# Performance work log

Measured on AMD Instinct MI355X. Metric: run time of the kernel, lower is better.

The kernel has to match this reference:

```python
import jax, jax.numpy as jnp
import numpy as np

N_SRC, N_DST, E, D, H = 100000, 10000, 320000, 128, 128
LN_EPS = 1e-5


def setup_inputs() -> dict:
    key = jax.random.key(0)
    ks = jax.random.split(key, 12)
    h_src = jax.random.normal(ks[0], (N_SRC, D), jnp.float32)
    h_dst = jax.random.normal(ks[1], (N_DST, D), jnp.float32)
    s_emb = jax.random.normal(ks[2], (N_DST, D), jnp.float32)
    edge_weight = jax.random.uniform(ks[3], (E,), jnp.float32)
    src_idx = jax.random.randint(ks[4], (E,), 0, N_SRC)
    dst_idx = jnp.sort(jax.random.randint(ks[5], (E,), 0, N_DST))
    # session_attention: Linear(2D->H, no bias) -> tanh -> Linear(H->1, no bias)
    W1 = jax.random.normal(ks[6], (2 * D, H), jnp.float32) / np.sqrt(2 * D)
    w2 = jax.random.normal(ks[7], (H,), jnp.float32) / np.sqrt(H)
    # output_proj: Linear(2D->D) with bias
    Wo = jax.random.normal(ks[8], (2 * D, D), jnp.float32) / np.sqrt(2 * D)
    bo = jnp.zeros((D,), jnp.float32)
    gamma = jnp.ones((D,), jnp.float32)
    beta = jnp.zeros((D,), jnp.float32)
    return {"h_src": h_src, "h_dst": h_dst, "s_emb": s_emb,
            "edge_weight": edge_weight, "src_idx": src_idx, "dst_idx": dst_idx,
            "W1": W1, "w2": w2, "Wo": Wo, "bo": bo, "gamma": gamma, "beta": beta}


def reference(h_src, h_dst, s_emb, edge_weight, src_idx, dst_idx, W1, w2, Wo, bo, gamma, beta):
    d = h_src.shape[1]
    # concat([h_src[src], s_emb[dst]]) @ W1 == h_src[src] @ W1[:d] + s_emb[dst] @ W1[d:]
    # project per-node first (cheaper than per-edge concat matmul)
    p_src = h_src @ W1[:d]          # [N_src, H]
    p_dst = s_emb @ W1[d:]          # [N_dst, H]
    raw = jnp.tanh(p_src[src_idx] + p_dst[dst_idx]) @ w2   # [E]
    raw = raw * edge_weight
    # edge_softmax: segment softmax over incoming edges of each dst node
    seg_max = jax.ops.segment_max(raw, dst_idx, num_segments=h_dst.shape[0])
    seg_max = jnp.where(jnp.isfinite(seg_max), seg_max, 0.0)  # handle degree-0 dsts
    ex = jnp.exp(raw - seg_max[dst_idx])
    den = jax.ops.segment_sum(ex, dst_idx, num_segments=h_dst.shape[0])
    attn = ex / den[dst_idx]                                 # [E]
    # u_mul_e + sum: weighted gather-scatter aggregation
    h_global = jax.ops.segment_sum(h_src[src_idx] * attn[:, None], dst_idx,
                                   num_segments=h_dst.shape[0])  # [N_dst, D]
    # output_proj on concat([h_dst, h_global])
    out = h_dst @ Wo[:d] + h_global @ Wo[d:] + bo
    # residual + layer norm (dropout = identity in eval)
    x = h_dst + out
    mu = jnp.mean(x, axis=-1, keepdims=True)
    var = jnp.mean((x - mu) ** 2, axis=-1, keepdims=True)
    y = (x - mu) / jnp.sqrt(var + LN_EPS) * gamma + beta
    return (y, attn[:, None])
```

## Files before the change

### kernel.cpp

```cpp
#include <hip/hip_runtime.h>
#include <math.h>

#define D128 128
#define SCAPW 256

typedef unsigned int uint32;
typedef unsigned short ushort_t;
typedef short bf16x8 __attribute__((ext_vector_type(8)));
typedef float f32x4 __attribute__((ext_vector_type(4)));
typedef float f32x2 __attribute__((ext_vector_type(2)));

__device__ __forceinline__ ushort_t bf16_of(float x) {
  uint32 u = __float_as_uint(x);
  return (ushort_t)((u + 0x7fffu + ((u >> 16) & 1u)) >> 16);
}
__device__ __forceinline__ uint32 pack_bf2(float x, float y) {
  uint32 bx = __float_as_uint(x);
  uint32 by = __float_as_uint(y);
  bx = (bx + 0x7fffu + ((bx >> 16) & 1u)) >> 16;
  by = (by + 0x7fffu + ((by >> 16) & 1u)) & 0xffff0000u;
  return bx | by;
}
__device__ __forceinline__ float bf_lo(uint32 u) { return __uint_as_float(u << 16); }
__device__ __forceinline__ float bf_hi(uint32 u) { return __uint_as_float(u & 0xffff0000u); }

__device__ __forceinline__ float fast_tanh(float x) {
  float e = __expf(2.0f * x);
  float r = __builtin_amdgcn_rcpf(1.0f + e);
  return fmaf(-2.0f, r, 1.0f);
}

__device__ __forceinline__ uint32 pack_fp8x4(float a, float b, float c, float d) {
  int u = __builtin_amdgcn_cvt_pk_fp8_f32(a, b, 0, false);
  u = __builtin_amdgcn_cvt_pk_fp8_f32(c, d, u, true);
  return (uint32)u;
}

__global__ __launch_bounds__(256) void prep_all(
    const float* __restrict__ h_src, const float* __restrict__ s_emb,
    const float* __restrict__ h_dst,
    const float* __restrict__ W1, const float* __restrict__ Wo,
    const int* __restrict__ dst_idx,
    uint32* __restrict__ h_src_bf, uint32* __restrict__ s_emb_bf,
    uint32* __restrict__ h_dst_bf, uint32* __restrict__ h_src_f8,
    ushort_t* __restrict__ Wfrag, ushort_t* __restrict__ Wo_frag,
    int* __restrict__ off,
    int n_src_el, int n_dst_el, int E, int N, int nb_conv) {
  const int b = blockIdx.x;
  const int tid = threadIdx.x;
  if (b < nb_conv) {
    int i = (b * 256 + tid) * 8;
    if (i < n_src_el) {
      float4 a = *(const float4*)(h_src + i);
      float4 c = *(const float4*)(h_src + i + 4);
      uint4 p;
      p.x = pack_bf2(a.x, a.y);
      p.y = pack_bf2(a.z, a.w);
      p.z = pack_bf2(c.x, c.y);
      p.w = pack_bf2(c.z, c.w);
      *(uint4*)(h_src_bf + (i >> 1)) = p;
      uint2 q;
      q.x = pack_fp8x4(a.x, a.y, a.z, a.w);
      q.y = pack_fp8x4(c.x, c.y, c.z, c.w);
      *(uint2*)(h_src_f8 + (i >> 2)) = q;
    } else if (i < n_src_el + 2 * n_dst_el) {
      const float* src;
      uint32* dst;
      if (i < n_src_el + n_dst_el) {
        src = s_emb + (i - n_src_el); dst = s_emb_bf + ((i - n_src_el) >> 1);
      } else {
        src = h_dst + (i - n_src_el - n_dst_el);
        dst = h_dst_bf + ((i - n_src_el - n_dst_el) >> 1);
      }
      float4 a = *(const float4*)src;
      float4 c = *(const float4*)(src + 4);
      uint4 p;
      p.x = pack_bf2(a.x, a.y);
      p.y = pack_bf2(a.z, a.w);
      p.z = pack_bf2(c.x, c.y);
      p.w = pack_bf2(c.z, c.w);
      *(uint4*)dst = p;
    }
  } else if (b < nb_conv + 16) {
    int t = (b - nb_conv) * 256 + tid;
    int lane = t & 63;
    int kc = (t >> 6) & 3;
    int nt = (t >> 8) & 7;
    int h = (t >> 11) & 1;
    int m = lane & 15;
    int quad = lane >> 4;
    int krow = h * D128 + kc * 32 + quad * 8;
    int ncol = nt * 16 + m;
    ushort_t fr[8];
#pragma unroll
    for (int j = 0; j < 8; j++) fr[j] = bf16_of(W1[(size_t)(krow + j) * D128 + ncol]);
    *(uint4*)(Wfrag + (size_t)t * 8) = *(const uint4*)fr;
  } else if (b < nb_conv + 32) {
    int t = (b - nb_conv - 16) * 256 + tid;
    int lane = t & 63;
    int kc = (t >> 6) & 7;
    int nt = (t >> 9) & 7;
    int m = lane & 15;
    int quad = lane >> 4;
    int krow = kc * 32 + quad * 8;
    int ncol = nt * 16 + m;
    ushort_t fr[8];
#pragma unroll
    for (int j = 0; j < 8; j++) fr[j] = bf16_of(Wo[(size_t)(krow + j) * D128 + ncol]);
    *(uint4*)(Wo_frag + (size_t)t * 8) = *(const uint4*)fr;
  } else {
    int e = (b - nb_conv - 32) * 256 + tid;
    if (e >= E) return;
    int d = dst_idx[e];
    int dprev = (e == 0) ? -1 : dst_idx[e - 1];
    for (int v = dprev + 1; v <= d; v++) off[v] = e;
    if (e == E - 1) {
      for (int v = d + 1; v <= N; v++) off[v] = E;
    }
  }
}

__global__ __launch_bounds__(256) void gemm_mfma(
    const ushort_t* __restrict__ Xa, const ushort_t* __restrict__ Xb,
    const ushort_t* __restrict__ Wfrag,
    uint32* __restrict__ Pa, uint32* __restrict__ Pb,
    int Ma, int Mb, int nblk_a) {
  __shared__ uint32 Ys8[128][36];
  const int blk = blockIdx.x;
  const ushort_t* X;
  const bf16x8* Wf;
  uint32* P;
  int M, row0;
  if (blk < nblk_a) { X = Xa; P = Pa; Wf = (const bf16x8*)Wfrag;           M = Ma; row0 = blk * 128; }
  else              { X = Xb; P = Pb; Wf = (const bf16x8*)(Wfrag + 16384); M = Mb; row0 = (blk - nblk_a) * 128; }

  const int tid = threadIdx.x;
  const int wave = tid >> 6;
  const int lane = tid & 63;
  const int m = lane & 15;
  const int quad = lane >> 4;

  const int ra0 = min(row0 + wave * 32 + m, M - 1);
  const int ra1 = min(row0 + wave * 32 + 16 + m, M - 1);

  f32x4 acc[2][8];
#pragma unroll
  for (int st = 0; st < 2; st++)
#pragma unroll
    for (int nt = 0; nt < 8; nt++) acc[st][nt] = (f32x4){0.f, 0.f, 0.f, 0.f};

#pragma unroll
  for (int kc = 0; kc < 4; kc++) {
    bf16x8 x0 = *(const bf16x8*)(X + (size_t)ra0 * D128 + kc * 32 + quad * 8);
    bf16x8 x1 = *(const bf16x8*)(X + (size_t)ra1 * D128 + kc * 32 + quad * 8);
#pragma unroll
    for (int nt = 0; nt < 8; nt++) {
      bf16x8 wf = Wf[(nt * 4 + kc) * 64 + lane];
      acc[0][nt] = __builtin_amdgcn_mfma_f32_16x16x32_bf16(wf, x0, acc[0][nt], 0, 0, 0);
      acc[1][nt] = __builtin_amdgcn_mfma_f32_16x16x32_bf16(wf, x1, acc[1][nt], 0, 0, 0);
    }
  }

#pragma unroll
  for (int st = 0; st < 2; st++)
#pragma unroll
    for (int nt = 0; nt < 8; nt++)
      Ys8[wave * 32 + st * 16 + m][nt * 4 + quad] =
          pack_fp8x4(acc[st][nt][0], acc[st][nt][1], acc[st][nt][2], acc[st][nt][3]);
  __syncthreads();

#pragma unroll
  for (int it = 0; it < 4; it++) {
    int f = tid + 256 * it;
    int row = f >> 3;
    int cu = (f & 7) * 4;
    int grow = row0 + row;
    if (grow < M) *(uint4*)(P + (size_t)grow * 32 + cu) = *(const uint4*)(&Ys8[row][cu]);
  }
}

__global__ __launch_bounds__(256) void attn_agg_kernel(
    const uint32* __restrict__ p_src_f8, const uint32* __restrict__ p_dst_f8,
    const float* __restrict__ w2, const float* __restrict__ ew,
    const int* __restrict__ src_idx, const int* __restrict__ off,
    const uint32* __restrict__ h_src_f8,
    float* __restrict__ attn_out, uint32* __restrict__ h_glob_bf, int N_dst) {
  const int tid = threadIdx.x;
  const int wv = tid >> 6;
  const int lane = tid & 63;
  const int v = blockIdx.x * 4 + wv;

  __shared__ float sex[4][SCAPW];
  __shared__ int ssrc[4][SCAPW];
  if (v >= N_dst) return;

  const int lo = off[v], hi = off[v + 1];
  const int deg = hi - lo;
  const int sub = lane & 15;
  const int eg = lane >> 4;
  const bool fast = (deg <= SCAPW);

  float4 wA = *(const float4*)(w2 + sub * 8);
  float4 wB = *(const float4*)(w2 + sub * 8 + 4);
  uint2 pdu = *(const uint2*)(p_dst_f8 + (size_t)v * 32 + sub * 2);
  f32x2 pd0 = __builtin_amdgcn_cvt_pk_f32_fp8(pdu.x, false);
  f32x2 pd1 = __builtin_amdgcn_cvt_pk_f32_fp8(pdu.x, true);
  f32x2 pd2 = __builtin_amdgcn_cvt_pk_f32_fp8(pdu.y, false);
  f32x2 pd3 = __builtin_amdgcn_cvt_pk_f32_fp8(pdu.y, true);

  float den = 0.f;
  for (int base = 0; base < deg; base += 4) {
    const int ei = base + eg;
    float ex = 0.f;
    if (ei < deg) {
      const int e = lo + ei;
      const int s = src_idx[e];
      const float ewv = ew[e];
      uint2 us = *(const uint2*)(p_src_f8 + (size_t)s * 32 + sub * 2);
      f32x2 a0 = __builtin_amdgcn_cvt_pk_f32_fp8(us.x, false);
      f32x2 a1 = __builtin_amdgcn_cvt_pk_f32_fp8(us.x, true);
      f32x2 a2 = __builtin_amdgcn_cvt_pk_f32_fp8(us.y, false);
      f32x2 a3 = __builtin_amdgcn_cvt_pk_f32_fp8(us.y, true);
      float sc;
      sc = fast_tanh(a0.x + pd0.x) * wA.x;
      sc = fmaf(fast_tanh(a0.y + pd0.y), wA.y, sc);
      sc = fmaf(fast_tanh(a1.x + pd1.x), wA.z, sc);
      sc = fmaf(fast_tanh(a1.y + pd1.y), wA.w, sc);
      sc = fmaf(fast_tanh(a2.x + pd2.x), wB.x, sc);
      sc = fmaf(fast_tanh(a2.y + pd2.y), wB.y, sc);
      sc = fmaf(fast_tanh(a3.x + pd3.x), wB.z, sc);
      sc = fmaf(fast_tanh(a3.y + pd3.y), wB.w, sc);
#pragma unroll
      for (int o = 1; o <= 8; o <<= 1) sc += __shfl_xor(sc, o, 64);
      ex = __expf(sc * ewv);
      if (sub == 0) {
        if (fast) { sex[wv][ei] = ex; ssrc[wv][ei] = s; }
        else attn_out[lo + ei] = ex;
      }
    }
    den += (sub == 0) ? ex : 0.f;
  }
#pragma unroll
  for (int o = 1; o <= 32; o <<= 1) den += __shfl_xor(den, o, 64);
  const float inv = (deg > 0) ? 1.0f / den : 0.0f;

  const int c4 = lane & 31;
  const int hw = lane >> 5;
  float a0 = 0.f, a1 = 0.f, a2 = 0.f, a3 = 0.f;

  if (fast) {
    const int pad = (deg + 15) & ~15;
    for (int i = deg + lane; i < pad; i += 64) { sex[wv][i] = 0.f; ssrc[wv][i] = 0; }
    for (int i = lane; i < deg; i += 64) attn_out[lo + i] = sex[wv][i] * inv;
    for (int b = 0; b < pad; b += 16) {
#pragma unroll
      for (int j = 0; j < 8; j++) {
        const int idx = b + j * 2 + hw;
        float ex = sex[wv][idx];
        int s = ssrc[wv][idx];
        uint32 u = h_src_f8[(size_t)s * 32 + c4];
        f32x2 h0 = __builtin_amdgcn_cvt_pk_f32_fp8(u, false);
        f32x2 h1 = __builtin_amdgcn_cvt_pk_f32_fp8(u, true);
        a0 = fmaf(ex, h0.x, a0);
        a1 = fmaf(ex, h0.y, a1);
        a2 = fmaf(ex, h1.x, a2);
        a3 = fmaf(ex, h1.y, a3);
      }
    }
  } else {
    for (int b = 0; b < deg; b += 16) {
#pragma unroll
      for (int j = 0; j < 8; j++) {
        const int idx = b + j * 2 + hw;
        float ex = 0.f;
        int s = 0;
        if (idx < deg) { ex = attn_out[lo + idx]; s = src_idx[lo + idx]; }
        uint32 u = h_src_f8[(size_t)s * 32 + c4];
        f32x2 h0 = __builtin_amdgcn_cvt_pk_f32_fp8(u, false);
        f32x2 h1 = __builtin_amdgcn_cvt_pk_f32_fp8(u, true);
        a0 = fmaf(ex, h0.x, a0);
        a1 = fmaf(ex, h0.y, a1);
        a2 = fmaf(ex, h1.x, a2);
        a3 = fmaf(ex, h1.y, a3);
      }
    }
    for (int i = lane; i < deg; i += 64) attn_out[lo + i] *= inv;
  }

  a0 += __shfl_xor(a0, 32, 64);
  a1 += __shfl_xor(a1, 32, 64);
  a2 += __shfl_xor(a2, 32, 64);
  a3 += __shfl_xor(a3, 32, 64);
  if (hw == 0) {
    uint2 o;
    o.x = pack_bf2(a0 * inv, a1 * inv);
    o.y = pack_bf2(a2 * inv, a3 * inv);
    *(uint2*)(h_glob_bf + (size_t)v * 64 + c4 * 2) = o;
  }
}

__global__ __launch_bounds__(128) void out_mfma_ln(
    const ushort_t* __restrict__ h_dst_bf, const ushort_t* __restrict__ h_glob_bf,
    const ushort_t* __restrict__ Wo_frag,
    const float* __restrict__ h_dst, const float* __restrict__ bo,
    const float* __restrict__ gamma, const float* __restrict__ beta,
    float* __restrict__ y, int N) {
  __shared__ float sbo[128], sgam[128], sbet[128];
  const int tid = threadIdx.x;
  if (tid < 128) { sbo[tid] = bo[tid]; sgam[tid] = gamma[tid]; sbet[tid] = beta[tid]; }
  __syncthreads();

  const int w = tid >> 6;
  const int lane = tid & 63;
  const int m = lane & 15;
  const int quad = lane >> 4;
  const int row0 = blockIdx.x * 32 + w * 16;
  const int ra = min(row0 + m, N - 1);
  const bf16x8* Wf = (const bf16x8*)Wo_frag;

  f32x4 acc[8];
#pragma unroll
  for (int nt = 0; nt < 8; nt++) acc[nt] = (f32x4){0.f, 0.f, 0.f, 0.f};

#pragma unroll
  for (int kc = 0; kc < 8; kc++) {
    const ushort_t* X = (kc < 4) ? h_dst_bf : h_glob_bf;
    const int kk = kc & 3;
    bf16x8 a = *(const bf16x8*)(X + (size_t)ra * D128 + kk * 32 + quad * 8);
#pragma unroll
    for (int nt = 0; nt < 8; nt++) {
      bf16x8 bfr = Wf[(nt * 8 + kc) * 64 + lane];
      acc[nt] = __builtin_amdgcn_mfma_f32_16x16x32_bf16(a, bfr, acc[nt], 0, 0, 0);
    }
  }

#pragma unroll
  for (int r = 0; r < 4; r++) {
    const int grow = row0 + quad * 4 + r;
    const int gr = min(grow, N - 1);
    float x[8];
    float s1 = 0.f, s2 = 0.f;
#pragma unroll
    for (int nt = 0; nt < 8; nt++) {
      float hd = h_dst[(size_t)gr * D128 + nt * 16 + m];
      float xv = hd + acc[nt][r] + sbo[nt * 16 + m];
      x[nt] = xv;
      s1 += xv;
      s2 = fmaf(xv, xv, s2);
    }
#pragma unroll
    for (int o = 1; o <= 8; o <<= 1) {
      s1 += __shfl_xor(s1, o, 64);
      s2 += __shfl_xor(s2, o, 64);
    }
    float mu = s1 * (1.0f / 128.0f);
    float var = s2 * (1.0f / 128.0f) - mu * mu;
    float rstd = __builtin_amdgcn_rcpf(sqrtf(var + 1e-5f));
    if (grow < N) {
#pragma unroll
      for (int nt = 0; nt < 8; nt++) {
        int c = nt * 16 + m;
        y[(size_t)grow * D128 + c] = (x[nt] - mu) * rstd * sgam[c] + sbet[c];
      }
    }
  }
}

extern "C" void kernel_launch(void* const* d_in, const int* in_sizes, int n_in,
                              void* d_out, int out_size, void* d_ws, size_t ws_size,
                              hipStream_t stream) {
  const float* h_src = (const float*)d_in[0];
  const float* h_dst = (const float*)d_in[1];
  const float* s_emb = (const float*)d_in[2];
  const float* ew    = (const float*)d_in[3];
  const int* src_idx = (const int*)d_in[4];
  const int* dst_idx = (const int*)d_in[5];
  const float* W1    = (const float*)d_in[6];
  const float* w2    = (const float*)d_in[7];
  const float* Wo    = (const float*)d_in[8];
  const float* bo    = (const float*)d_in[9];
  const float* gamma = (const float*)d_in[10];
  const float* beta  = (const float*)d_in[11];

  const int N_src = in_sizes[0] / D128;
  const int N_dst = in_sizes[1] / D128;
  const int E = in_sizes[3];

  float* out_y = (float*)d_out;
  float* out_attn = out_y + (size_t)N_dst * D128;

  uint32* p_src_f8 = (uint32*)d_ws;
  uint32* p_dst_f8 = p_src_f8 + (size_t)N_src * 32;
  uint32* h_src_f8 = p_dst_f8 + (size_t)N_dst * 32;
  uint32* h_src_bf = h_src_f8 + (size_t)N_src * 32;
  uint32* h_dst_bf = h_src_bf + (size_t)N_src * 64;
  uint32* h_glob_bf = h_dst_bf + (size_t)N_dst * 64;
  uint32* s_emb_bf = h_glob_bf + (size_t)N_dst * 64;
  int* seg_off = (int*)(s_emb_bf + (size_t)N_dst * 64);
  ushort_t* Wfrag = (ushort_t*)(seg_off + N_dst + 1 + 3);
  ushort_t* Wo_frag = Wfrag + 32768;

  const int n_src_el = N_src * D128;
  const int n_dst_el = N_dst * D128;
  const int n_conv_el = n_src_el + 2 * n_dst_el;
  const int nblk_a = (N_src + 127) / 128;
  const int nblk_b = (N_dst + 127) / 128;
  const int nb_conv = (n_conv_el / 8 + 255) / 256;
  const int nb_seg = (E + 255) / 256;

  prep_all<<<nb_conv + 32 + nb_seg, 256, 0, stream>>>(
      h_src, s_emb, h_dst, W1, Wo, dst_idx,
      h_src_bf, s_emb_bf, h_dst_bf, h_src_f8, Wfrag, Wo_frag, seg_off,
      n_src_el, n_dst_el, E, N_dst, nb_conv);
  gemm_mfma<<<nblk_a + nblk_b, 256, 0, stream>>>(
      (const ushort_t*)h_src_bf, (const ushort_t*)s_emb_bf, Wfrag,
      p_src_f8, p_dst_f8, N_src, N_dst, nblk_a);
  attn_agg_kernel<<<(N_dst + 3) / 4, 256, 0, stream>>>(
      p_src_f8, p_dst_f8, w2, ew, src_idx, seg_off, h_src_f8, out_attn,
      h_glob_bf, N_dst);
  out_mfma_ln<<<(N_dst + 31) / 32, 128, 0, stream>>>(
      (const ushort_t*)h_dst_bf, (const ushort_t*)h_glob_bf, Wo_frag,
      h_dst, bo, gamma, beta, out_y, N_dst);
}
```

Baseline: 175.9 us.

## Fuse fp32-to-bf16/fp8 conversion into GEMM and output kernels

Removes the separate conversion pass in prep_all that wrote bf16 copies of h_src, s_emb and h_dst and an fp8 copy of h_src. The GEMM now reads fp32 inputs directly, converts them to bf16 in registers, and also emits the fp8 h_src copy. The output projection converts h_dst on the fly. This removes a full read-write round trip over about 60 MB of activations, in exchange for twice the input bytes per GEMM load and conversion ALU work inside the MFMA kernels.

```diff
diff --git a/kernel.cpp b/kernel.cpp
--- a/kernel.cpp
+++ b/kernel.cpp
@@ -21,8 +21,6 @@
   by = (by + 0x7fffu + ((by >> 16) & 1u)) & 0xffff0000u;
   return bx | by;
 }
-__device__ __forceinline__ float bf_lo(uint32 u) { return __uint_as_float(u << 16); }
-__device__ __forceinline__ float bf_hi(uint32 u) { return __uint_as_float(u & 0xffff0000u); }
 
 __device__ __forceinline__ float fast_tanh(float x) {
   float e = __expf(2.0f * x);
@@ -36,53 +34,24 @@
   return (uint32)u;
 }
 
+__device__ __forceinline__ bf16x8 bf16x8_of(float4 a, float4 c) {
+  union { uint4 u; bf16x8 h; } r;
+  r.u.x = pack_bf2(a.x, a.y);
+  r.u.y = pack_bf2(a.z, a.w);
+  r.u.z = pack_bf2(c.x, c.y);
+  r.u.w = pack_bf2(c.z, c.w);
+  return r.h;
+}
+
 __global__ __launch_bounds__(256) void prep_all(
-    const float* __restrict__ h_src, const float* __restrict__ s_emb,
-    const float* __restrict__ h_dst,
     const float* __restrict__ W1, const float* __restrict__ Wo,
     const int* __restrict__ dst_idx,
-    uint32* __restrict__ h_src_bf, uint32* __restrict__ s_emb_bf,
-    uint32* __restrict__ h_dst_bf, uint32* __restrict__ h_src_f8,
     ushort_t* __restrict__ Wfrag, ushort_t* __restrict__ Wo_frag,
-    int* __restrict__ off,
-    int n_src_el, int n_dst_el, int E, int N, int nb_conv) {
+    int* __restrict__ off, int E, int N) {
   const int b = blockIdx.x;
   const int tid = threadIdx.x;
-  if (b < nb_conv) {
-    int i = (b * 256 + tid) * 8;
-    if (i < n_src_el) {
-      float4 a = *(const float4*)(h_src + i);
-      float4 c = *(const float4*)(h_src + i + 4);
-      uint4 p;
-      p.x = pack_bf2(a.x, a.y);
-      p.y = pack_bf2(a.z, a.w);
-      p.z = pack_bf2(c.x, c.y);
-      p.w = pack_bf2(c.z, c.w);
-      *(uint4*)(h_src_bf + (i >> 1)) = p;
-      uint2 q;
-      q.x = pack_fp8x4(a.x, a.y, a.z, a.w);
-      q.y = pack_fp8x4(c.x, c.y, c.z, c.w);
-      *(uint2*)(h_src_f8 + (i >> 2)) = q;
-    } else if (i < n_src_el + 2 * n_dst_el) {
-      const float* src;
-      uint32* dst;
-      if (i < n_src_el + n_dst_el) {
-        src = s_emb + (i - n_src_el); dst = s_emb_bf + ((i - n_src_el) >> 1);
-      } else {
-        src = h_dst + (i - n_src_el - n_dst_el);
-        dst = h_dst_bf + ((i - n_src_el - n_dst_el) >> 1);
-      }
-      float4 a = *(const float4*)src;
-      float4 c = *(const float4*)(src + 4);
-      uint4 p;
-      p.x = pack_bf2(a.x, a.y);
-      p.y = pack_bf2(a.z, a.w);
-      p.z = pack_bf2(c.x, c.y);
-      p.w = pack_bf2(c.z, c.w);
-      *(uint4*)dst = p;
-    }
-  } else if (b < nb_conv + 16) {
-    int t = (b - nb_conv) * 256 + tid;
+  if (b < 16) {
+    int t = b * 256 + tid;
     int lane = t & 63;
     int kc = (t >> 6) & 3;
     int nt = (t >> 8) & 7;
@@ -95,8 +64,8 @@
 #pragma unroll
     for (int j = 0; j < 8; j++) fr[j] = bf16_of(W1[(size_t)(krow + j) * D128 + ncol]);
     *(uint4*)(Wfrag + (size_t)t * 8) = *(const uint4*)fr;
-  } else if (b < nb_conv + 32) {
-    int t = (b - nb_conv - 16) * 256 + tid;
+  } else if (b < 32) {
+    int t = (b - 16) * 256 + tid;
     int lane = t & 63;
     int kc = (t >> 6) & 7;
     int nt = (t >> 9) & 7;
@@ -109,7 +78,7 @@
     for (int j = 0; j < 8; j++) fr[j] = bf16_of(Wo[(size_t)(krow + j) * D128 + ncol]);
     *(uint4*)(Wo_frag + (size_t)t * 8) = *(const uint4*)fr;
   } else {
-    int e = (b - nb_conv - 32) * 256 + tid;
+    int e = (b - 32) * 256 + tid;
     if (e >= E) return;
     int d = dst_idx[e];
     int dprev = (e == 0) ? -1 : dst_idx[e - 1];
@@ -121,18 +90,23 @@
 }
 
 __global__ __launch_bounds__(256) void gemm_mfma(
-    const ushort_t* __restrict__ Xa, const ushort_t* __restrict__ Xb,
+    const float* __restrict__ Xa, const float* __restrict__ Xb,
     const ushort_t* __restrict__ Wfrag,
     uint32* __restrict__ Pa, uint32* __restrict__ Pb,
+    uint32* __restrict__ x_f8,
     int Ma, int Mb, int nblk_a) {
   __shared__ uint32 Ys8[128][36];
   const int blk = blockIdx.x;
-  const ushort_t* X;
+  const float* X;
   const bf16x8* Wf;
   uint32* P;
   int M, row0;
-  if (blk < nblk_a) { X = Xa; P = Pa; Wf = (const bf16x8*)Wfrag;           M = Ma; row0 = blk * 128; }
-  else              { X = Xb; P = Pb; Wf = (const bf16x8*)(Wfrag + 16384); M = Mb; row0 = (blk - nblk_a) * 128; }
+  bool emit8;
+  if (blk < nblk_a) {
+    X = Xa; P = Pa; Wf = (const bf16x8*)Wfrag;           M = Ma; row0 = blk * 128; emit8 = true;
+  } else {
+    X = Xb; P = Pb; Wf = (const bf16x8*)(Wfrag + 16384); M = Mb; row0 = (blk - nblk_a) * 128; emit8 = false;
+  }
 
   const int tid = threadIdx.x;
   const int wave = tid >> 6;
@@ -151,8 +125,23 @@
 
 #pragma unroll
   for (int kc = 0; kc < 4; kc++) {
-    bf16x8 x0 = *(const bf16x8*)(X + (size_t)ra0 * D128 + kc * 32 + quad * 8);
-    bf16x8 x1 = *(const bf16x8*)(X + (size_t)ra1 * D128 + kc * 32 + quad * 8);
+    const float* p0 = X + (size_t)ra0 * D128 + kc * 32 + quad * 8;
+    const float* p1 = X + (size_t)ra1 * D128 + kc * 32 + quad * 8;
+    float4 a0 = *(const float4*)p0;
+    float4 a1 = *(const float4*)(p0 + 4);
+    float4 b0 = *(const float4*)p1;
+    float4 b1 = *(const float4*)(p1 + 4);
+    bf16x8 x0 = bf16x8_of(a0, a1);
+    bf16x8 x1 = bf16x8_of(b0, b1);
+    if (emit8) {
+      uint2 q;
+      q.x = pack_fp8x4(a0.x, a0.y, a0.z, a0.w);
+      q.y = pack_fp8x4(a1.x, a1.y, a1.z, a1.w);
+      *(uint2*)(x_f8 + (size_t)ra0 * 32 + kc * 8 + quad * 2) = q;
+      q.x = pack_fp8x4(b0.x, b0.y, b0.z, b0.w);
+      q.y = pack_fp8x4(b1.x, b1.y, b1.z, b1.w);
+      *(uint2*)(x_f8 + (size_t)ra1 * 32 + kc * 8 + quad * 2) = q;
+    }
 #pragma unroll
     for (int nt = 0; nt < 8; nt++) {
       bf16x8 wf = Wf[(nt * 4 + kc) * 64 + lane];
@@ -300,9 +289,9 @@
 }
 
 __global__ __launch_bounds__(128) void out_mfma_ln(
-    const ushort_t* __restrict__ h_dst_bf, const ushort_t* __restrict__ h_glob_bf,
+    const float* __restrict__ h_dst, const ushort_t* __restrict__ h_glob_bf,
     const ushort_t* __restrict__ Wo_frag,
-    const float* __restrict__ h_dst, const float* __restrict__ bo,
+    const float* __restrict__ bo,
     const float* __restrict__ gamma, const float* __restrict__ beta,
     float* __restrict__ y, int N) {
   __shared__ float sbo[128], sgam[128], sbet[128];
@@ -324,9 +313,15 @@
 
 #pragma unroll
   for (int kc = 0; kc < 8; kc++) {
-    const ushort_t* X = (kc < 4) ? h_dst_bf : h_glob_bf;
-    const int kk = kc & 3;
-    bf16x8 a = *(const bf16x8*)(X + (size_t)ra * D128 + kk * 32 + quad * 8);
+    bf16x8 a;
+    if (kc < 4) {
+      const float* p = h_dst + (size_t)ra * D128 + kc * 32 + quad * 8;
+      float4 f0 = *(const float4*)p;
+      float4 f1 = *(const float4*)(p + 4);
+      a = bf16x8_of(f0, f1);
+    } else {
+      a = *(const bf16x8*)(h_glob_bf + (size_t)ra * D128 + (kc & 3) * 32 + quad * 8);
+    }
 #pragma unroll
     for (int nt = 0; nt < 8; nt++) {
       bf16x8 bfr = Wf[(nt * 8 + kc) * 64 + lane];
@@ -392,33 +387,23 @@
   uint32* p_src_f8 = (uint32*)d_ws;
   uint32* p_dst_f8 = p_src_f8 + (size_t)N_src * 32;
   uint32* h_src_f8 = p_dst_f8 + (size_t)N_dst * 32;
-  uint32* h_src_bf = h_src_f8 + (size_t)N_src * 32;
-  uint32* h_dst_bf = h_src_bf + (size_t)N_src * 64;
-  uint32* h_glob_bf = h_dst_bf + (size_t)N_dst * 64;
-  uint32* s_emb_bf = h_glob_bf + (size_t)N_dst * 64;
-  int* seg_off = (int*)(s_emb_bf + (size_t)N_dst * 64);
+  uint32* h_glob_bf = h_src_f8 + (size_t)N_src * 32;
+  int* seg_off = (int*)(h_glob_bf + (size_t)N_dst * 64);
   ushort_t* Wfrag = (ushort_t*)(seg_off + N_dst + 1 + 3);
   ushort_t* Wo_frag = Wfrag + 32768;
 
-  const int n_src_el = N_src * D128;
-  const int n_dst_el = N_dst * D128;
-  const int n_conv_el = n_src_el + 2 * n_dst_el;
   const int nblk_a = (N_src + 127) / 128;
   const int nblk_b = (N_dst + 127) / 128;
-  const int nb_conv = (n_conv_el / 8 + 255) / 256;
   const int nb_seg = (E + 255) / 256;
 
-  prep_all<<<nb_conv + 32 + nb_seg, 256, 0, stream>>>(
-      h_src, s_emb, h_dst, W1, Wo, dst_idx,
-      h_src_bf, s_emb_bf, h_dst_bf, h_src_f8, Wfrag, Wo_frag, seg_off,
-      n_src_el, n_dst_el, E, N_dst, nb_conv);
+  prep_all<<<32 + nb_seg, 256, 0, stream>>>(
+      W1, Wo, dst_idx, Wfrag, Wo_frag, seg_off, E, N_dst);
   gemm_mfma<<<nblk_a + nblk_b, 256, 0, stream>>>(
-      (const ushort_t*)h_src_bf, (const ushort_t*)s_emb_bf, Wfrag,
-      p_src_f8, p_dst_f8, N_src, N_dst, nblk_a);
+      h_src, s_emb, Wfrag, p_src_f8, p_dst_f8, h_src_f8, N_src, N_dst, nblk_a);
   attn_agg_kernel<<<(N_dst + 3) / 4, 256, 0, stream>>>(
       p_src_f8, p_dst_f8, w2, ew, src_idx, seg_off, h_src_f8, out_attn,
       h_glob_bf, N_dst);
   out_mfma_ln<<<(N_dst + 31) / 32, 128, 0, stream>>>(
-      (const ushort_t*)h_dst_bf, (const ushort_t*)h_glob_bf, Wo_frag,
-      h_dst, bo, gamma, beta, out_y, N_dst);
-}
+      h_dst, (const ushort_t*)h_glob_bf, Wo_frag,
+      bo, gamma, beta, out_y, N_dst);
+}
```

After: 172.6 us. Within noise of the previous version (-1.9%).
